# Optimization experiments

Hardware: AMD Instinct MI355X
Metric: run time of the kernel (lower is better)

The kernel has to match this reference:

```python
import jax, jax.numpy as jnp
import numpy as np

SIGMA = 8.0          # self.sigama
IGNORE_THR = 0.5     # self.ignore_threshold

def _clog(p):
    # torch BCELoss clamps log at -100
    return jnp.clip(jnp.log(jnp.clip(p, 1e-12, 1.0)), -100.0, 0.0)

def _bce(p, t):
    return -(t * _clog(p) + (1.0 - t) * _clog(1.0 - p))

def _smooth_l1(a, b):
    d = jnp.abs(a - b)
    return jnp.where(d < 1.0, 0.5 * d * d, d - 0.5)

def setup_inputs() -> dict:
    key = jax.random.key(0)
    k1, k2, k3, k4, k5 = jax.random.split(key, 5)
    bs, T, C, H, W = 32, 50, 80, 76, 76
    inp = jax.random.normal(k1, (bs, 5 + C, H, W), dtype=jnp.float32) * 0.5
    cls = jax.random.randint(k2, (bs, T, 1), 0, C).astype(jnp.float32)
    xy = jax.random.uniform(k3, (bs, T, 2), minval=0.02, maxval=0.98)
    wh = jax.random.uniform(k4, (bs, T, 2), minval=0.02, maxval=0.30)
    targets = jnp.concatenate([cls, xy, wh], -1)
    # variable number of valid targets per image; zero rows are skipped by the loss
    nvalid = jax.random.randint(k5, (bs,), 5, T)
    tmask = (jnp.arange(T)[None, :] < nvalid[:, None]).astype(jnp.float32)
    targets = targets * tmask[..., None]
    return {"input": inp, "targets": targets}

def reference(input, targets):
    bs, A, H, W = input.shape
    C = A - 5
    T = targets.shape[1]
    dt = input.dtype

    pred = jnp.transpose(input, (0, 2, 3, 1))  # [bs,H,W,A]
    x = jax.nn.sigmoid(pred[..., 0])
    y = jax.nn.sigmoid(pred[..., 1])
    w = pred[..., 2]
    h = pred[..., 3]
    conf = jax.nn.sigmoid(pred[..., 4])
    pred_cls = jax.nn.sigmoid(pred[..., 5:])

    gx_grid = jnp.arange(W, dtype=dt)[None, None, :]
    gy_grid = jnp.arange(H, dtype=dt)[None, :, None]
    pred_boxes = jnp.stack([x + gx_grid, y + gy_grid,
                            jnp.exp(w) * SIGMA, jnp.exp(h) * SIGMA], -1)
    pb = jax.lax.stop_gradient(pred_boxes)  # .detach() in original

    # ---- vectorized get_target ----
    valid = jnp.sum(targets, -1) != 0                      # [bs,T]
    gx = targets[..., 1] * W
    gy = targets[..., 2] * H
    gw = targets[..., 3] * W
    gh = targets[..., 4] * H
    gi = jnp.clip(gx.astype(jnp.int32), 0, W - 1)
    gj = jnp.clip(gy.astype(jnp.int32), 0, H - 1)
    cells = gj * W + gi
    # duplicate-cell skip: a target is dropped if an earlier VALID target hit the same cell
    tri = jnp.tril(jnp.ones((T, T), bool), -1)             # [t, t'] true iff t' < t
    dup = jnp.any((cells[:, :, None] == cells[:, None, :]) & valid[:, None, :] & tri[None], -1)
    eff = valid & ~dup
    efff = eff.astype(dt)
    n_obj = jnp.sum(efff)

    # IoU of every effective gt box vs all grid pred boxes (center format)
    g = jnp.stack([gx, gy, gw, gh], -1)[:, :, None, :]      # [bs,T,1,4]
    p = pb.reshape(bs, 1, H * W, 4)                         # [bs,1,HW,4]
    gx1, gy1 = g[..., 0] - g[..., 2] / 2, g[..., 1] - g[..., 3] / 2
    gx2, gy2 = g[..., 0] + g[..., 2] / 2, g[..., 1] + g[..., 3] / 2
    px1, py1 = p[..., 0] - p[..., 2] / 2, p[..., 1] - p[..., 3] / 2
    px2, py2 = p[..., 0] + p[..., 2] / 2, p[..., 1] + p[..., 3] / 2
    iw = jnp.clip(jnp.minimum(gx2, px2) - jnp.maximum(gx1, px1), 0.0)
    ih = jnp.clip(jnp.minimum(gy2, py2) - jnp.maximum(gy1, py1), 0.0)
    inter = iw * ih
    iou = inter / (g[..., 2] * g[..., 3] + p[..., 2] * p[..., 3] - inter + 1e-16)
    iou = iou.reshape(bs, T, H, W)
    ignore = jnp.any((iou >= IGNORE_THR) & eff[:, :, None, None], 1)  # [bs,H,W]

    bidx = jnp.broadcast_to(jnp.arange(bs)[:, None], (bs, T))
    def scat(vals):
        return jnp.zeros((bs, H, W), dt).at[bidx, gj, gi].add(efff * vals)
    mask = scat(jnp.ones_like(efff))
    scales = scat(2.0 - targets[..., 3] * targets[..., 4])
    tx = scat(gx - gi.astype(dt))
    ty = scat(gy - gj.astype(dt))
    tw = scat(jnp.log(gw / SIGMA + 1e-16))
    th = scat(jnp.log(gh / SIGMA + 1e-16))
    cls_idx = jnp.clip(targets[..., 0].astype(jnp.int32), 0, C - 1)
    tcls = jnp.zeros((bs, H, W, C), dt).at[bidx, gj, gi, cls_idx].add(efff)
    noobj_mask = jnp.where(ignore | (mask > 0), 0.0, 1.0).astype(dt)

    # ---- losses (all lambdas are 1) ----
    loss_x = (mask * scales * _bce(x, tx)).sum() / n_obj
    loss_y = (mask * scales * _bce(y, ty)).sum() / n_obj
    loss_w = (mask * scales * _smooth_l1(w, tw)).sum() / n_obj
    loss_h = (mask * scales * _smooth_l1(h, th)).sum() / n_obj
    loss_conf = (_bce(conf * mask, mask).sum()
                 + 0.5 * _bce(noobj_mask * conf, jnp.zeros_like(conf)).sum()) / n_obj
    loss_tcls = jnp.where(jnp.sum(tcls) > 0,
                          (mask[..., None] * _bce(pred_cls, tcls)).sum() / n_obj,
                          jnp.zeros((), dt))
    loss = loss_x + loss_y + loss_w + loss_h + loss_conf + loss_tcls
    return (loss, loss_x, loss_y, loss_w, loss_h, loss_conf, loss_tcls)
```

## Files before the change

### kernel.cpp

```cpp
#include <hip/hip_runtime.h>
#include <math.h>

#define BS 32
#define NT 50
#define NC 80
#define H 76
#define W 76
#define HW (H*W)
#define NA (5+NC)
#define SIGMA 8.0f
#define YBLK 23
#define NBLK (BS*YBLK)

__device__ __forceinline__ float clog_(float p){
    p = fminf(fmaxf(p, 1e-12f), 1.0f);
    float l = logf(p);
    return fminf(fmaxf(l, -100.0f), 0.0f);
}

__device__ __forceinline__ float sigmoid_(float v){
    return 1.0f / (1.0f + expf(-v));
}

__global__ __launch_bounds__(256) void yolo_main(
    const float* __restrict__ input,
    const float* __restrict__ targets,
    float*       __restrict__ partials,
    int*         __restrict__ counts)
{
    const int b   = blockIdx.x;
    const int yb  = blockIdx.y;
    const int tid = threadIdx.x;
    const int bid = b * YBLK + yb;

    __shared__ float4 s_box[NT];
    __shared__ int    s_cellc[NT];
    __shared__ float4 s_rest[NT];
    __shared__ float2 s_sc[NT];
    __shared__ int    s_cell[NT];
    __shared__ unsigned char s_valid[NT];
    __shared__ int    s_count;

    if (tid == 0) s_count = 0;

    float cls=0.f, xx=0.f, yy=0.f, ww=0.f, hh=0.f;
    bool valid = false;
    int cell0 = 0;
    if (tid < NT){
        const float* p = targets + ((size_t)b*NT + tid)*5;
        cls = p[0]; xx = p[1]; yy = p[2]; ww = p[3]; hh = p[4];
        valid = ((cls + xx + yy + ww + hh) != 0.0f);
        float gx = xx * (float)W, gy = yy * (float)H;
        int gi = min(max((int)gx, 0), W-1);
        int gj = min(max((int)gy, 0), H-1);
        cell0 = gj*W + gi;
        s_cell[tid]  = cell0;
        s_valid[tid] = valid ? 1 : 0;
    }
    __syncthreads();
    if (tid < NT && valid){
        bool dup = false;
        for (int u = 0; u < tid; ++u)
            if (s_valid[u] && s_cell[u] == cell0) dup = true;
        if (!dup){
            int idx = atomicAdd(&s_count, 1);
            float gx = xx*(float)W, gy = yy*(float)H;
            float gw = ww*(float)W, gh = hh*(float)H;
            int gi = min(max((int)gx, 0), W-1);
            int gj = min(max((int)gy, 0), H-1);
            s_box[idx]  = make_float4(gx - gw*0.5f, gy - gh*0.5f,
                                      gx + gw*0.5f, gy + gh*0.5f);
            s_cellc[idx]= cell0;
            s_rest[idx] = make_float4(gx - (float)gi, gy - (float)gj,
                                      logf(gw/SIGMA + 1e-16f),
                                      logf(gh/SIGMA + 1e-16f));
            s_sc[idx]   = make_float2(2.0f - ww*hh,
                                      (float)min(max((int)cls, 0), NC-1));
        }
    }
    __syncthreads();
    const int nb = s_count;

    float lx=0.f, ly=0.f, lw=0.f, lh=0.f, lc=0.f, lt=0.f;

    const int cellLo = yb * 256;
    const int cellHi = (cellLo + 256 < HW) ? cellLo + 256 : HW;
    const float* binp = input + (size_t)b*NA*HW;

    for (int t = 0; t < nb; ++t){
        int q = s_cellc[t];
        if (q >= cellLo && q < cellHi && tid < NC){
            float pc = sigmoid_(binp[(size_t)(5+tid)*HW + q]);
            int cidx = (int)s_sc[t].y;
            lt += (tid == cidx) ? -clog_(pc) : -clog_(1.f - pc);
        }
    }

    const int cell = cellLo + tid;
    if (cell < HW){
        const float* base = binp + cell;
        float vx = base[0];
        float vy = base[HW];
        float vw = base[2*HW];
        float vh = base[3*HW];
        float vc = base[4*HW];
        float x    = sigmoid_(vx);
        float y    = sigmoid_(vy);
        float conf = sigmoid_(vc);
        int i = cell / W, j = cell - i*W;
        float pw = expf(vw) * SIGMA;
        float ph = expf(vh) * SIGMA;
        float px = x + (float)j;
        float py = y + (float)i;
        float px1 = px - pw*0.5f, px2 = px + pw*0.5f;
        float py1 = py - ph*0.5f, py2 = py + ph*0.5f;
        float parea = pw * ph;

        bool ignore = false;
        int myt = -1;
        for (int t = 0; t < nb; ++t){
            float4 bx = s_box[t];
            float garea = (bx.z - bx.x) * (bx.w - bx.y);
            float iw = fminf(bx.z, px2) - fmaxf(bx.x, px1);
            float ih = fminf(bx.w, py2) - fmaxf(bx.y, py1);
            iw = fmaxf(iw, 0.f); ih = fmaxf(ih, 0.f);
            float inter = iw * ih;
            ignore = ignore || (inter >= 0.5f*(garea + parea - inter + 1e-16f));
            if (s_cellc[t] == cell) myt = t;
        }

        if (myt >= 0){
            float4 r = s_rest[myt];
            float scale = s_sc[myt].x;
            lx = scale * (-(r.x*clog_(x) + (1.f-r.x)*clog_(1.f-x)));
            ly = scale * (-(r.y*clog_(y) + (1.f-r.y)*clog_(1.f-y)));
            float dw = fabsf(vw - r.z);
            lw = scale * (dw < 1.f ? 0.5f*dw*dw : dw - 0.5f);
            float dh = fabsf(vh - r.w);
            lh = scale * (dh < 1.f ? 0.5f*dh*dh : dh - 0.5f);
            lc = -clog_(conf);
        } else if (!ignore){
            lc = 0.5f * (-clog_(1.0f - conf));
        }
    }

    #pragma unroll
    for (int off = 32; off > 0; off >>= 1){
        lx += __shfl_down(lx, off);
        ly += __shfl_down(ly, off);
        lw += __shfl_down(lw, off);
        lh += __shfl_down(lh, off);
        lc += __shfl_down(lc, off);
        lt += __shfl_down(lt, off);
    }
    __shared__ float s_red[4*6];
    if ((tid & 63) == 0){
        int wv = tid >> 6;
        s_red[wv*6+0] = lx; s_red[wv*6+1] = ly; s_red[wv*6+2] = lw;
        s_red[wv*6+3] = lh; s_red[wv*6+4] = lc; s_red[wv*6+5] = lt;
    }
    __syncthreads();
    if (tid < 6){
        float v = s_red[tid] + s_red[6+tid] + s_red[12+tid] + s_red[18+tid];
        partials[tid*NBLK + bid] = v;
    }
    if (yb == 0 && tid == 0) counts[b] = nb;
}

__global__ __launch_bounds__(256) void finalize_k(
    const float* __restrict__ partials,
    const int*   __restrict__ counts,
    float*       __restrict__ out)
{
    int tid = threadIdx.x;
    float loc[6] = {0,0,0,0,0,0};
    for (int k = tid; k < NBLK; k += 256){
        #pragma unroll
        for (int j = 0; j < 6; ++j) loc[j] += partials[j*NBLK + k];
    }
    float nloc = (tid < BS) ? (float)counts[tid] : 0.f;

    #pragma unroll
    for (int off = 32; off > 0; off >>= 1){
        #pragma unroll
        for (int j = 0; j < 6; ++j) loc[j] += __shfl_down(loc[j], off);
        nloc += __shfl_down(nloc, off);
    }
    __shared__ float s_red[4*7];
    if ((tid & 63) == 0){
        int wv = tid >> 6;
        #pragma unroll
        for (int j = 0; j < 6; ++j) s_red[wv*7+j] = loc[j];
        s_red[wv*7+6] = nloc;
    }
    __syncthreads();
    if (tid == 0){
        float s[7];
        #pragma unroll
        for (int j = 0; j < 7; ++j)
            s[j] = s_red[j] + s_red[7+j] + s_red[14+j] + s_red[21+j];
        float n = s[6];
        float inv = (n > 0.f) ? (1.0f / n) : 0.0f;
        float lx = s[0]*inv, ly = s[1]*inv, lw = s[2]*inv, lh = s[3]*inv;
        float lconf = s[4]*inv;
        float ltcls = (n > 0.f) ? s[5]*inv : 0.0f;
        out[0] = lx + ly + lw + lh + lconf + ltcls;
        out[1] = lx;
        out[2] = ly;
        out[3] = lw;
        out[4] = lh;
        out[5] = lconf;
        out[6] = ltcls;
    }
}

extern "C" void kernel_launch(void* const* d_in, const int* in_sizes, int n_in,
                              void* d_out, int out_size, void* d_ws, size_t ws_size,
                              hipStream_t stream) {
    const float* input   = (const float*)d_in[0];
    const float* targets = (const float*)d_in[1];
    float* out = (float*)d_out;

    float* partials = (float*)d_ws;
    int*   counts   = (int*)((char*)d_ws + 6*NBLK*sizeof(float));

    dim3 grid(BS, YBLK);
    yolo_main<<<grid, dim3(256), 0, stream>>>(input, targets, partials, counts);
    finalize_k<<<1, dim3(256), 0, stream>>>(partials, counts, out);
}
```

Measured before the change: 108.1 us.

## Precompute target boxes in separate prep kernel and overlap input loads

Moves target parsing, duplicate detection and box precomputation out of every main-kernel block into a small prep kernel that runs once per image and writes packed float4 records to workspace. The main kernel then copies those records into shared memory and issues its per-cell input loads before the barrier, so global loads overlap the target setup. Ground-truth area is also precomputed. The cost is an extra kernel launch and a round trip through global memory. Cell indices are stored as floats, which is exact for the values used here.

```diff
diff --git a/kernel.cpp b/kernel.cpp
--- a/kernel.cpp
+++ b/kernel.cpp
@@ -22,45 +22,36 @@
     return 1.0f / (1.0f + expf(-v));
 }
 
-__global__ __launch_bounds__(256) void yolo_main(
-    const float* __restrict__ input,
+__global__ __launch_bounds__(64) void prep_k(
     const float* __restrict__ targets,
-    float*       __restrict__ partials,
+    float4*      __restrict__ tdata,
     int*         __restrict__ counts)
 {
-    const int b   = blockIdx.x;
-    const int yb  = blockIdx.y;
-    const int tid = threadIdx.x;
-    const int bid = b * YBLK + yb;
-
-    __shared__ float4 s_box[NT];
-    __shared__ int    s_cellc[NT];
-    __shared__ float4 s_rest[NT];
-    __shared__ float2 s_sc[NT];
-    __shared__ int    s_cell[NT];
+    const int b = blockIdx.x;
+    const int t = threadIdx.x;
+    __shared__ int s_cell[NT];
     __shared__ unsigned char s_valid[NT];
-    __shared__ int    s_count;
-
-    if (tid == 0) s_count = 0;
+    __shared__ int s_count;
+    if (t == 0) s_count = 0;
 
     float cls=0.f, xx=0.f, yy=0.f, ww=0.f, hh=0.f;
     bool valid = false;
     int cell0 = 0;
-    if (tid < NT){
-        const float* p = targets + ((size_t)b*NT + tid)*5;
+    if (t < NT){
+        const float* p = targets + ((size_t)b*NT + t)*5;
         cls = p[0]; xx = p[1]; yy = p[2]; ww = p[3]; hh = p[4];
         valid = ((cls + xx + yy + ww + hh) != 0.0f);
         float gx = xx * (float)W, gy = yy * (float)H;
         int gi = min(max((int)gx, 0), W-1);
         int gj = min(max((int)gy, 0), H-1);
         cell0 = gj*W + gi;
-        s_cell[tid]  = cell0;
-        s_valid[tid] = valid ? 1 : 0;
-    }
-    __syncthreads();
-    if (tid < NT && valid){
+        s_cell[t]  = cell0;
+        s_valid[t] = valid ? 1 : 0;
+    }
+    __syncthreads();
+    if (t < NT && valid){
         bool dup = false;
-        for (int u = 0; u < tid; ++u)
+        for (int u = 0; u < t; ++u)
             if (s_valid[u] && s_cell[u] == cell0) dup = true;
         if (!dup){
             int idx = atomicAdd(&s_count, 1);
@@ -68,42 +59,69 @@
             float gw = ww*(float)W, gh = hh*(float)H;
             int gi = min(max((int)gx, 0), W-1);
             int gj = min(max((int)gy, 0), H-1);
-            s_box[idx]  = make_float4(gx - gw*0.5f, gy - gh*0.5f,
-                                      gx + gw*0.5f, gy + gh*0.5f);
-            s_cellc[idx]= cell0;
-            s_rest[idx] = make_float4(gx - (float)gi, gy - (float)gj,
-                                      logf(gw/SIGMA + 1e-16f),
-                                      logf(gh/SIGMA + 1e-16f));
-            s_sc[idx]   = make_float2(2.0f - ww*hh,
-                                      (float)min(max((int)cls, 0), NC-1));
-        }
-    }
-    __syncthreads();
-    const int nb = s_count;
+            float4* d = tdata + ((size_t)b*NT + idx)*3;
+            d[0] = make_float4(gx - gw*0.5f, gy - gh*0.5f,
+                               gx + gw*0.5f, gy + gh*0.5f);
+            d[1] = make_float4(gx - (float)gi, gy - (float)gj,
+                               logf(gw/SIGMA + 1e-16f),
+                               logf(gh/SIGMA + 1e-16f));
+            d[2] = make_float4(2.0f - ww*hh,
+                               (float)min(max((int)cls, 0), NC-1),
+                               (float)cell0,
+                               gw * gh);
+        }
+    }
+    __syncthreads();
+    if (t == 0) counts[b] = s_count;
+}
+
+__global__ __launch_bounds__(256) void yolo_main(
+    const float*  __restrict__ input,
+    const float4* __restrict__ tdata,
+    const int*    __restrict__ counts,
+    float*        __restrict__ partials)
+{
+    const int b   = blockIdx.x;
+    const int yb  = blockIdx.y;
+    const int tid = threadIdx.x;
+    const int bid = b * YBLK + yb;
+
+    __shared__ float4 s_t4[NT*3];
+    __shared__ int s_nb;
+
+    if (tid < NT*3) s_t4[tid] = tdata[(size_t)b*NT*3 + tid];
+    if (tid == 0)   s_nb = counts[b];
+
+    const int cellLo = yb * 256;
+    const int cell   = cellLo + tid;
+    const float* binp = input + (size_t)b*NA*HW;
+    float vx=0.f, vy=0.f, vw=0.f, vh=0.f, vc=0.f;
+    const bool incell = (cell < HW);
+    if (incell){
+        const float* base = binp + cell;
+        vx = base[0];
+        vy = base[HW];
+        vw = base[2*HW];
+        vh = base[3*HW];
+        vc = base[4*HW];
+    }
+    __syncthreads();
+    const int nb = s_nb;
 
     float lx=0.f, ly=0.f, lw=0.f, lh=0.f, lc=0.f, lt=0.f;
 
-    const int cellLo = yb * 256;
     const int cellHi = (cellLo + 256 < HW) ? cellLo + 256 : HW;
-    const float* binp = input + (size_t)b*NA*HW;
-
     for (int t = 0; t < nb; ++t){
-        int q = s_cellc[t];
+        float4 meta = s_t4[3*t+2];
+        int q = (int)meta.z;
         if (q >= cellLo && q < cellHi && tid < NC){
             float pc = sigmoid_(binp[(size_t)(5+tid)*HW + q]);
-            int cidx = (int)s_sc[t].y;
+            int cidx = (int)meta.y;
             lt += (tid == cidx) ? -clog_(pc) : -clog_(1.f - pc);
         }
     }
 
-    const int cell = cellLo + tid;
-    if (cell < HW){
-        const float* base = binp + cell;
-        float vx = base[0];
-        float vy = base[HW];
-        float vw = base[2*HW];
-        float vh = base[3*HW];
-        float vc = base[4*HW];
+    if (incell){
         float x    = sigmoid_(vx);
         float y    = sigmoid_(vy);
         float conf = sigmoid_(vc);
@@ -119,19 +137,19 @@
         bool ignore = false;
         int myt = -1;
         for (int t = 0; t < nb; ++t){
-            float4 bx = s_box[t];
-            float garea = (bx.z - bx.x) * (bx.w - bx.y);
+            float4 bx   = s_t4[3*t];
+            float4 meta = s_t4[3*t+2];
             float iw = fminf(bx.z, px2) - fmaxf(bx.x, px1);
             float ih = fminf(bx.w, py2) - fmaxf(bx.y, py1);
             iw = fmaxf(iw, 0.f); ih = fmaxf(ih, 0.f);
             float inter = iw * ih;
-            ignore = ignore || (inter >= 0.5f*(garea + parea - inter + 1e-16f));
-            if (s_cellc[t] == cell) myt = t;
+            ignore = ignore || (inter >= 0.5f*(meta.w + parea - inter + 1e-16f));
+            if ((int)meta.z == cell) myt = t;
         }
 
         if (myt >= 0){
-            float4 r = s_rest[myt];
-            float scale = s_sc[myt].x;
+            float4 r    = s_t4[3*myt+1];
+            float scale = s_t4[3*myt+2].x;
             lx = scale * (-(r.x*clog_(x) + (1.f-r.x)*clog_(1.f-x)));
             ly = scale * (-(r.y*clog_(y) + (1.f-r.y)*clog_(1.f-y)));
             float dw = fabsf(vw - r.z);
@@ -164,7 +182,6 @@
         float v = s_red[tid] + s_red[6+tid] + s_red[12+tid] + s_red[18+tid];
         partials[tid*NBLK + bid] = v;
     }
-    if (yb == 0 && tid == 0) counts[b] = nb;
 }
 
 __global__ __launch_bounds__(256) void finalize_k(
@@ -221,10 +238,14 @@
     const float* targets = (const float*)d_in[1];
     float* out = (float*)d_out;
 
-    float* partials = (float*)d_ws;
-    int*   counts   = (int*)((char*)d_ws + 6*NBLK*sizeof(float));
+    float4* tdata    = (float4*)d_ws;
+    float*  partials = (float*)((char*)d_ws + 76800);
+    int*    counts   = (int*)((char*)d_ws + 76800 + 6*NBLK*sizeof(float));
+
+    prep_k<<<dim3(BS), dim3(64), 0, stream>>>(targets, tdata, counts);
 
     dim3 grid(BS, YBLK);
-    yolo_main<<<grid, dim3(256), 0, stream>>>(input, targets, partials, counts);
+    yolo_main<<<grid, dim3(256), 0, stream>>>(input, tdata, counts, partials);
+
     finalize_k<<<1, dim3(256), 0, stream>>>(partials, counts, out);
 }
```

Measured after the change: 109.0 us. About the same (+0.9%).
